# Kernel optimization log

Hardware: AMD Instinct MI355X
Metric: run time of the kernel (lower is better)

Reference implementation:

```python
import jax, jax.numpy as jnp
import numpy as np

B, S, D, H = 2, 2048, 1024, 16
HD = D // H  # 64

def setup_inputs() -> dict:
    key = jax.random.key(0)
    k1, k2, k3 = jax.random.split(key, 3)
    x = jax.random.normal(k1, (B, S, D), dtype=jnp.float32)
    w_qkv = jax.random.normal(k2, (D, 3 * D), dtype=jnp.float32) * 0.02
    w_out = jax.random.normal(k3, (D, D), dtype=jnp.float32) * 0.02
    b_out = jnp.zeros((D,), dtype=jnp.float32)
    return {"x": x, "w_qkv": w_qkv, "w_out": w_out, "b_out": b_out}

def reference(x, w_qkv, w_out, b_out):
    # fused qkv projection (no bias)
    qkv = jnp.einsum('bsd,de->bse', x, w_qkv)            # [B,S,3D]
    q, k, v = jnp.split(qkv, 3, axis=-1)                 # each [B,S,D]
    def split_heads(t):
        return t.reshape(B, S, H, HD).transpose(0, 2, 1, 3)  # [B,H,S,HD]
    q, k, v = split_heads(q), split_heads(k), split_heads(v)
    scores = jnp.einsum('bhqd,bhkd->bhqk', q, k) / jnp.sqrt(jnp.float32(HD))
    probs = jax.nn.softmax(scores, axis=-1)              # [B,H,S,S]
    attn = jnp.einsum('bhqk,bhkd->bhqd', probs, v)       # [B,H,S,HD]
    attn = attn.transpose(0, 2, 1, 3).reshape(B, S, D)   # [B,S,D]
    out = jnp.einsum('bsd,de->bse', attn, w_out) + b_out
    return out
```

## Files before the change

### kernel.cpp

```cpp
#include <hip/hip_runtime.h>
#include <stdint.h>

#define B_  2
#define S_  2048
#define D_  1024
#define H_  16
#define HD_ 64
#define KVT 128
#define NT  (S_ / KVT)

typedef __attribute__((ext_vector_type(8))) short short8;
typedef __attribute__((ext_vector_type(4))) float f32x4;

__device__ inline unsigned short f2bf(float f) {
  union { float f; unsigned int i; } u; u.f = f;
  unsigned int r = u.i + 0x7FFFu + ((u.i >> 16) & 1u);
  return (unsigned short)(r >> 16);
}

__device__ inline uint32_t cvtpk_bf16(float lo, float hi) {
  uint32_t r;
  asm("v_cvt_pk_bf16_f32 %0, %1, %2" : "=v"(r) : "v"(lo), "v"(hi));
  return r;
}

__device__ inline float fexp2(float x) {
  float r;
  asm("v_exp_f32 %0, %1" : "=v"(r) : "v"(x));
  return r;
}

__device__ inline void gload16(const void* g, void* l) {
  __builtin_amdgcn_global_load_lds(
      (const __attribute__((address_space(1))) void*)g,
      (__attribute__((address_space(3))) void*)l,
      16, 0, 0);
}

__global__ void cast_kernel(const float* __restrict__ in,
                            unsigned short* __restrict__ out, int n) {
  int i = (blockIdx.x * blockDim.x + threadIdx.x) * 4;
  if (i >= n) return;
  float4 v = *(const float4*)(in + i);
  union { unsigned short s[4]; uint2 v; } o;
  o.s[0] = f2bf(v.x); o.s[1] = f2bf(v.y); o.s[2] = f2bf(v.z); o.s[3] = f2bf(v.w);
  *(uint2*)(out + i) = o.v;
}

__global__ void transpose_cast_kernel(const float* __restrict__ in,
                                      unsigned short* __restrict__ out,
                                      int R, int C) {
  __shared__ float tile[32][33];
  int bx = blockIdx.x, by = blockIdx.y;
  int tx = threadIdx.x, ty = threadIdx.y;
#pragma unroll
  for (int i = 0; i < 4; ++i)
    tile[ty + i * 8][tx] = in[(size_t)(by * 32 + ty + i * 8) * C + bx * 32 + tx];
  __syncthreads();
#pragma unroll
  for (int i = 0; i < 4; ++i)
    out[(size_t)(bx * 32 + ty + i * 8) * R + by * 32 + tx] = f2bf(tile[tx][ty + i * 8]);
}

__global__ __launch_bounds__(256, 3)
void gemm_qkv(const unsigned short* __restrict__ A,
              const unsigned short* __restrict__ Bt,
              unsigned short* __restrict__ qw,
              unsigned short* __restrict__ kw,
              unsigned short* __restrict__ vTw) {
  const int K = 1024;
  __shared__ __align__(16) unsigned short As[128 * 64];
  __shared__ __align__(16) unsigned short Bs[128 * 64];
  const int t  = threadIdx.x;
  const int w  = t >> 6, l = t & 63;
  const int lr = l & 15, lg = l >> 4;
  const int wr = w >> 1, wc = w & 1;
  const int bn = blockIdx.x, bm = blockIdx.y;

  const int srow = t >> 3;
  const int scol = 8 * ((t & 7) ^ (srow & 7));

  const unsigned short* Ab = A  + (size_t)(bm * 128 + srow) * K + scol;
  const unsigned short* Bb = Bt + (size_t)(bn * 128 + srow) * K + scol;

  f32x4 acc[4][4];
#pragma unroll
  for (int m = 0; m < 4; ++m)
#pragma unroll
    for (int n = 0; n < 4; ++n)
      acc[m][n] = (f32x4){0.f, 0.f, 0.f, 0.f};

  for (int kt = 0; kt < K; kt += 64) {
#pragma unroll
    for (int i = 0; i < 4; ++i) {
      gload16(Ab + (size_t)i * 32 * K + kt, &As[(size_t)(i * 256 + t) * 8]);
      gload16(Bb + (size_t)i * 32 * K + kt, &Bs[(size_t)(i * 256 + t) * 8]);
    }
    __syncthreads();
#pragma unroll
    for (int ks = 0; ks < 2; ++ks) {
      short8 af[4], bf[4];
#pragma unroll
      for (int m = 0; m < 4; ++m) {
        int row = wr * 64 + m * 16 + lr;
        af[m] = *(const short8*)&As[row * 64 + ((ks * 32 + lg * 8) ^ ((row & 7) * 8))];
      }
#pragma unroll
      for (int n = 0; n < 4; ++n) {
        int row = wc * 64 + n * 16 + lr;
        bf[n] = *(const short8*)&Bs[row * 64 + ((ks * 32 + lg * 8) ^ ((row & 7) * 8))];
      }
#pragma unroll
      for (int m = 0; m < 4; ++m)
#pragma unroll
        for (int n = 0; n < 4; ++n)
          acc[m][n] = __builtin_amdgcn_mfma_f32_16x16x32_bf16(af[m], bf[n], acc[m][n], 0, 0, 0);
    }
    __syncthreads();
  }

#pragma unroll
  for (int m = 0; m < 4; ++m)
#pragma unroll
    for (int n = 0; n < 4; ++n)
#pragma unroll
      for (int r = 0; r < 4; ++r) {
        float v = acc[m][n][r];
        int i = bm * 128 + wr * 64 + m * 16 + lg * 4 + r;
        int j = bn * 128 + wc * 64 + n * 16 + lr;
        int b = i >> 11, s = i & 2047;
        int part = j >> 10, rem = j & 1023, h = rem >> 6, hd = rem & 63;
        size_t bh = (size_t)(b * H_ + h);
        if (part == 0) {
          qw[(bh * S_ + s) * HD_ + hd] = f2bf(v * 0.1803368801f);
        } else if (part == 1) {
          kw[(bh * S_ + s) * HD_ + hd] = f2bf(v);
        } else {
          int s6 = s & 63;
          int sp = (s & ~63) | (s6 & 32) | (((s6 >> 2) & 3) << 3)
                 | (((s6 >> 4) & 1) << 2) | (s6 & 3);
          vTw[(bh * HD_ + hd) * S_ + sp] = f2bf(v);
        }
      }
}

__global__ __launch_bounds__(256)
void gemm_out(const unsigned short* __restrict__ A,
              const unsigned short* __restrict__ Bt,
              float* __restrict__ out,
              const float* __restrict__ bias) {
  const int K = 1024;
  __shared__ __align__(16) unsigned short As[128 * 64];
  __shared__ __align__(16) unsigned short Bs[64 * 64];
  const int t  = threadIdx.x;
  const int w  = t >> 6, l = t & 63;
  const int lr = l & 15, lg = l >> 4;
  const int wr = w >> 1, wc = w & 1;
  const int bn = blockIdx.x, bm = blockIdx.y;

  const int srow = t >> 3;
  const int scol = 8 * ((t & 7) ^ (srow & 7));

  const unsigned short* Ab = A  + (size_t)(bm * 128 + srow) * K + scol;
  const unsigned short* Bb = Bt + (size_t)(bn * 64 + srow) * K + scol;

  f32x4 acc[4][2];
#pragma unroll
  for (int m = 0; m < 4; ++m)
#pragma unroll
    for (int n = 0; n < 2; ++n)
      acc[m][n] = (f32x4){0.f, 0.f, 0.f, 0.f};

  for (int kt = 0; kt < K; kt += 64) {
#pragma unroll
    for (int i = 0; i < 4; ++i)
      gload16(Ab + (size_t)i * 32 * K + kt, &As[(size_t)(i * 256 + t) * 8]);
#pragma unroll
    for (int i = 0; i < 2; ++i)
      gload16(Bb + (size_t)i * 32 * K + kt, &Bs[(size_t)(i * 256 + t) * 8]);
    __syncthreads();
#pragma unroll
    for (int ks = 0; ks < 2; ++ks) {
      short8 af[4], bf[2];
#pragma unroll
      for (int m = 0; m < 4; ++m) {
        int row = wr * 64 + m * 16 + lr;
        af[m] = *(const short8*)&As[row * 64 + ((ks * 32 + lg * 8) ^ ((row & 7) * 8))];
      }
#pragma unroll
      for (int n = 0; n < 2; ++n) {
        int row = wc * 32 + n * 16 + lr;
        bf[n] = *(const short8*)&Bs[row * 64 + ((ks * 32 + lg * 8) ^ ((row & 7) * 8))];
      }
#pragma unroll
      for (int m = 0; m < 4; ++m)
#pragma unroll
        for (int n = 0; n < 2; ++n)
          acc[m][n] = __builtin_amdgcn_mfma_f32_16x16x32_bf16(af[m], bf[n], acc[m][n], 0, 0, 0);
    }
    __syncthreads();
  }

#pragma unroll
  for (int m = 0; m < 4; ++m)
#pragma unroll
    for (int n = 0; n < 2; ++n)
#pragma unroll
      for (int r = 0; r < 4; ++r) {
        int i = bm * 128 + wr * 64 + m * 16 + lg * 4 + r;
        int j = bn * 64 + wc * 32 + n * 16 + lr;
        out[(size_t)i * D_ + j] = acc[m][n][r] + bias[j];
      }
}

__global__ __launch_bounds__(256, 2)
void attn_kernel(const unsigned short* __restrict__ qw,
                 const unsigned short* __restrict__ kw,
                 const unsigned short* __restrict__ vTw,
                 unsigned short* __restrict__ attn) {
  __shared__ __align__(16) unsigned short Ks[2][KVT * 64];
  __shared__ __align__(16) unsigned short Vs[2][64 * KVT];

  const int t  = threadIdx.x;
  const int w  = t >> 6, l = t & 63;
  const int lr = l & 15, lg = l >> 4;

  const int bid = blockIdx.x;
  const int bh = (bid & 7) * 4 + ((bid >> 3) & 3);
  const int qt = bid >> 5;

  const int q0 = qt * 128 + w * 32;
  const unsigned short* Qb = qw  + (size_t)bh * S_ * HD_;
  const unsigned short* Kb = kw  + (size_t)bh * S_ * HD_;
  const unsigned short* Vb = vTw + (size_t)bh * HD_ * S_;

  const int krow = t >> 3, kcol = 8 * ((t & 7) ^ ((t >> 3) & 7));
  const int vrow = t >> 4, vcol = 8 * ((t & 15) ^ ((t >> 4) & 7));

  const short8 ones = {16256, 16256, 16256, 16256, 16256, 16256, 16256, 16256};
  const f32x4 FZERO = (f32x4){0.f, 0.f, 0.f, 0.f};

  short8 qf[2][2];
#pragma unroll
  for (int m = 0; m < 2; ++m)
#pragma unroll
    for (int ks = 0; ks < 2; ++ks)
      qf[m][ks] = *(const short8*)&Qb[(size_t)(q0 + m * 16 + lr) * HD_ + ks * 32 + lg * 8];

  f32x4 of[2][4];
  f32x4 osum[2];
  float mrun[2];
#pragma unroll
  for (int m = 0; m < 2; ++m) {
#pragma unroll
    for (int n = 0; n < 4; ++n) of[m][n] = FZERO;
    osum[m] = FZERO;
    mrun[m] = -1e30f;
  }

#pragma unroll
  for (int i = 0; i < 4; ++i) {
    gload16(Kb + (size_t)(i * 32 + krow) * HD_ + kcol, &Ks[0][(i * 256 + t) * 8]);
    gload16(Vb + (size_t)(i * 16 + vrow) * S_ + vcol,  &Vs[0][(i * 256 + t) * 8]);
  }
  __syncthreads();

  int cur = 0;
  for (int tt = 0; tt < NT; ++tt) {
    if (tt + 1 < NT) {
      const int kt = (tt + 1) * KVT;
#pragma unroll
      for (int i = 0; i < 4; ++i) {
        gload16(Kb + (size_t)(kt + i * 32 + krow) * HD_ + kcol, &Ks[cur ^ 1][(i * 256 + t) * 8]);
        gload16(Vb + (size_t)(i * 16 + vrow) * S_ + kt + vcol,  &Vs[cur ^ 1][(i * 256 + t) * 8]);
      }
    }

    f32x4 sfT[2][8];
    __builtin_amdgcn_s_setprio(1);
#pragma unroll
    for (int n = 0; n < 8; ++n) {
      int row = n * 16 + lr;
      short8 kf0 = *(const short8*)&Ks[cur][row * 64 + ((lg * 8) ^ ((row & 7) * 8))];
      sfT[0][n] = __builtin_amdgcn_mfma_f32_16x16x32_bf16(kf0, qf[0][0], FZERO, 0, 0, 0);
      sfT[1][n] = __builtin_amdgcn_mfma_f32_16x16x32_bf16(kf0, qf[1][0], FZERO, 0, 0, 0);
      short8 kf1 = *(const short8*)&Ks[cur][row * 64 + ((32 + lg * 8) ^ ((row & 7) * 8))];
      sfT[0][n] = __builtin_amdgcn_mfma_f32_16x16x32_bf16(kf1, qf[0][1], sfT[0][n], 0, 0, 0);
      sfT[1][n] = __builtin_amdgcn_mfma_f32_16x16x32_bf16(kf1, qf[1][1], sfT[1][n], 0, 0, 0);
    }
    __builtin_amdgcn_s_setprio(0);

    float mx[2];
    bool need = false;
#pragma unroll
    for (int m = 0; m < 2; ++m) {
      f32x4 cm = sfT[m][0];
#pragma unroll
      for (int n = 1; n < 8; ++n) {
        cm[0] = fmaxf(cm[0], sfT[m][n][0]);
        cm[1] = fmaxf(cm[1], sfT[m][n][1]);
        cm[2] = fmaxf(cm[2], sfT[m][n][2]);
        cm[3] = fmaxf(cm[3], sfT[m][n][3]);
      }
      float v = fmaxf(fmaxf(cm[0], cm[1]), fmaxf(cm[2], cm[3]));
      v = fmaxf(v, __shfl_xor(v, 16));
      v = fmaxf(v, __shfl_xor(v, 32));
      mx[m] = v;
      need = need || (v > mrun[m] + 10.0f);
    }
    if (__any(need)) {
#pragma unroll
      for (int m = 0; m < 2; ++m) {
        float mn = fmaxf(mrun[m], mx[m]);
        float al = fexp2(mrun[m] - mn);
        mrun[m] = mn;
#pragma unroll
        for (int n = 0; n < 4; ++n)
#pragma unroll
          for (int r = 0; r < 4; ++r) of[m][n][r] *= al;
#pragma unroll
        for (int r = 0; r < 4; ++r) osum[m][r] *= al;
      }
    }
    union { uint32_t u[4]; short8 v; } pb[2][4];
#pragma unroll
    for (int m = 0; m < 2; ++m) {
      float mm = mrun[m];
#pragma unroll
      for (int n = 0; n < 8; ++n) {
        sfT[m][n][0] = fexp2(sfT[m][n][0] - mm);
        sfT[m][n][1] = fexp2(sfT[m][n][1] - mm);
        sfT[m][n][2] = fexp2(sfT[m][n][2] - mm);
        sfT[m][n][3] = fexp2(sfT[m][n][3] - mm);
      }
#pragma unroll
      for (int kk = 0; kk < 4; ++kk) {
        pb[m][kk].u[0] = cvtpk_bf16(sfT[m][2 * kk][0],     sfT[m][2 * kk][1]);
        pb[m][kk].u[1] = cvtpk_bf16(sfT[m][2 * kk][2],     sfT[m][2 * kk][3]);
        pb[m][kk].u[2] = cvtpk_bf16(sfT[m][2 * kk + 1][0], sfT[m][2 * kk + 1][1]);
        pb[m][kk].u[3] = cvtpk_bf16(sfT[m][2 * kk + 1][2], sfT[m][2 * kk + 1][3]);
      }
    }

    __builtin_amdgcn_s_setprio(1);
#pragma unroll
    for (int nd = 0; nd < 4; ++nd)
#pragma unroll
      for (int kk = 0; kk < 4; ++kk) {
        int row = nd * 16 + lr;
        short8 vf = *(const short8*)&Vs[cur][row * 128 + ((kk * 32 + lg * 8) ^ ((row & 7) * 8))];
        of[0][nd] = __builtin_amdgcn_mfma_f32_16x16x32_bf16(vf, pb[0][kk].v, of[0][nd], 0, 0, 0);
        of[1][nd] = __builtin_amdgcn_mfma_f32_16x16x32_bf16(vf, pb[1][kk].v, of[1][nd], 0, 0, 0);
      }
#pragma unroll
    for (int m = 0; m < 2; ++m)
#pragma unroll
      for (int kk = 0; kk < 4; ++kk)
        osum[m] = __builtin_amdgcn_mfma_f32_16x16x32_bf16(ones, pb[m][kk].v, osum[m], 0, 0, 0);
    __builtin_amdgcn_s_setprio(0);

    __syncthreads();
    cur ^= 1;
  }

  const int b = bh >> 4, h = bh & 15;
#pragma unroll
  for (int m = 0; m < 2; ++m) {
    float inv = 1.0f / osum[m][0];
    int q = q0 + m * 16 + lr;
#pragma unroll
    for (int nd = 0; nd < 4; ++nd)
#pragma unroll
      for (int r = 0; r < 4; ++r)
        attn[((size_t)b * S_ + q) * D_ + h * 64 + nd * 16 + lg * 4 + r] =
            f2bf(of[m][nd][r] * inv);
  }
}

extern "C" void kernel_launch(void* const* d_in, const int* in_sizes, int n_in,
                              void* d_out, int out_size, void* d_ws, size_t ws_size,
                              hipStream_t stream) {
  const float* x     = (const float*)d_in[0];
  const float* w_qkv = (const float*)d_in[1];
  const float* w_out = (const float*)d_in[2];
  const float* b_out = (const float*)d_in[3];
  float* out = (float*)d_out;

  char* p = (char*)d_ws;
  unsigned short* xb    = (unsigned short*)p; p += (size_t)4096 * 1024 * 2;
  unsigned short* wqkvT = (unsigned short*)p; p += (size_t)3072 * 1024 * 2;
  unsigned short* woutT = (unsigned short*)p; p += (size_t)1024 * 1024 * 2;
  unsigned short* qws   = (unsigned short*)p; p += (size_t)B_ * H_ * S_ * HD_ * 2;
  unsigned short* kws   = (unsigned short*)p; p += (size_t)B_ * H_ * S_ * HD_ * 2;
  unsigned short* vTws  = (unsigned short*)p; p += (size_t)B_ * H_ * S_ * HD_ * 2;
  unsigned short* attnb = (unsigned short*)p; p += (size_t)4096 * 1024 * 2;

  cast_kernel<<<4096, 256, 0, stream>>>(x, xb, 4096 * 1024);
  dim3 tb(32, 8);
  transpose_cast_kernel<<<dim3(96, 32), tb, 0, stream>>>(w_qkv, wqkvT, 1024, 3072);
  transpose_cast_kernel<<<dim3(32, 32), tb, 0, stream>>>(w_out, woutT, 1024, 1024);

  gemm_qkv<<<dim3(24, 32), 256, 0, stream>>>(xb, wqkvT, qws, kws, vTws);

  attn_kernel<<<512, 256, 0, stream>>>(qws, kws, vTws, attnb);

  gemm_out<<<dim3(16, 32), 256, 0, stream>>>(attnb, woutT, out, b_out);
}
```

Measured before the change: 118.4 us.

## Load V fragments directly from global into registers instead of LDS

Drops the shared-memory double buffer for the transposed V tile. Each wave now loads its own V MFMA fragments straight from global memory at the start of each KV iteration. This halves LDS use and removes the async V copies, which may raise occupancy. The cost is that all four waves redundantly fetch the same V data, adds 16 short8 registers per thread, and exposes global-load latency that is only partly hidden behind the QK^T MFMAs. The row-max reduction is also rewritten as a per-lane chain.

```diff
diff --git a/kernel.cpp b/kernel.cpp
--- a/kernel.cpp
+++ b/kernel.cpp
@@ -219,7 +219,6 @@
                  const unsigned short* __restrict__ vTw,
                  unsigned short* __restrict__ attn) {
   __shared__ __align__(16) unsigned short Ks[2][KVT * 64];
-  __shared__ __align__(16) unsigned short Vs[2][64 * KVT];
 
   const int t  = threadIdx.x;
   const int w  = t >> 6, l = t & 63;
@@ -235,7 +234,6 @@
   const unsigned short* Vb = vTw + (size_t)bh * HD_ * S_;
 
   const int krow = t >> 3, kcol = 8 * ((t & 7) ^ ((t >> 3) & 7));
-  const int vrow = t >> 4, vcol = 8 * ((t & 15) ^ ((t >> 4) & 7));
 
   const short8 ones = {16256, 16256, 16256, 16256, 16256, 16256, 16256, 16256};
   const f32x4 FZERO = (f32x4){0.f, 0.f, 0.f, 0.f};
@@ -259,22 +257,26 @@
   }
 
 #pragma unroll
-  for (int i = 0; i < 4; ++i) {
+  for (int i = 0; i < 4; ++i)
     gload16(Kb + (size_t)(i * 32 + krow) * HD_ + kcol, &Ks[0][(i * 256 + t) * 8]);
-    gload16(Vb + (size_t)(i * 16 + vrow) * S_ + vcol,  &Vs[0][(i * 256 + t) * 8]);
-  }
   __syncthreads();
 
   int cur = 0;
   for (int tt = 0; tt < NT; ++tt) {
+    const int kt = tt * KVT;
     if (tt + 1 < NT) {
-      const int kt = (tt + 1) * KVT;
-#pragma unroll
-      for (int i = 0; i < 4; ++i) {
-        gload16(Kb + (size_t)(kt + i * 32 + krow) * HD_ + kcol, &Ks[cur ^ 1][(i * 256 + t) * 8]);
-        gload16(Vb + (size_t)(i * 16 + vrow) * S_ + kt + vcol,  &Vs[cur ^ 1][(i * 256 + t) * 8]);
-      }
-    }
+#pragma unroll
+      for (int i = 0; i < 4; ++i)
+        gload16(Kb + (size_t)(kt + KVT + i * 32 + krow) * HD_ + kcol,
+                &Ks[cur ^ 1][(i * 256 + t) * 8]);
+    }
+
+    short8 vr[4][4];
+#pragma unroll
+    for (int nd = 0; nd < 4; ++nd)
+#pragma unroll
+      for (int kk = 0; kk < 4; ++kk)
+        vr[nd][kk] = *(const short8*)&Vb[(size_t)(nd * 16 + lr) * S_ + kt + kk * 32 + lg * 8];
 
     f32x4 sfT[2][8];
     __builtin_amdgcn_s_setprio(1);
@@ -294,13 +296,14 @@
     bool need = false;
 #pragma unroll
     for (int m = 0; m < 2; ++m) {
-      f32x4 cm = sfT[m][0];
-#pragma unroll
-      for (int n = 1; n < 8; ++n) {
-        cm[0] = fmaxf(cm[0], sfT[m][n][0]);
-        cm[1] = fmaxf(cm[1], sfT[m][n][1]);
-        cm[2] = fmaxf(cm[2], sfT[m][n][2]);
-        cm[3] = fmaxf(cm[3], sfT[m][n][3]);
+      f32x4 cm;
+#pragma unroll
+      for (int j = 0; j < 4; ++j) {
+        float c = fmaxf(sfT[m][0][j], sfT[m][1][j]);
+        c = fmaxf(fmaxf(c, sfT[m][2][j]), sfT[m][3][j]);
+        c = fmaxf(fmaxf(c, sfT[m][4][j]), sfT[m][5][j]);
+        c = fmaxf(fmaxf(c, sfT[m][6][j]), sfT[m][7][j]);
+        cm[j] = c;
       }
       float v = fmaxf(fmaxf(cm[0], cm[1]), fmaxf(cm[2], cm[3]));
       v = fmaxf(v, __shfl_xor(v, 16));
@@ -347,10 +350,8 @@
     for (int nd = 0; nd < 4; ++nd)
 #pragma unroll
       for (int kk = 0; kk < 4; ++kk) {
-        int row = nd * 16 + lr;
-        short8 vf = *(const short8*)&Vs[cur][row * 128 + ((kk * 32 + lg * 8) ^ ((row & 7) * 8))];
-        of[0][nd] = __builtin_amdgcn_mfma_f32_16x16x32_bf16(vf, pb[0][kk].v, of[0][nd], 0, 0, 0);
-        of[1][nd] = __builtin_amdgcn_mfma_f32_16x16x32_bf16(vf, pb[1][kk].v, of[1][nd], 0, 0, 0);
+        of[0][nd] = __builtin_amdgcn_mfma_f32_16x16x32_bf16(vr[nd][kk], pb[0][kk].v, of[0][nd], 0, 0, 0);
+        of[1][nd] = __builtin_amdgcn_mfma_f32_16x16x32_bf16(vr[nd][kk], pb[1][kk].v, of[1][nd], 0, 0, 0);
       }
 #pragma unroll
     for (int m = 0; m < 2; ++m)
```

Measured after the change: 141.1 us. 1.19x slower.
